# Kernel optimization log

Hardware: AMD Instinct MI355X
Metric: run time of the kernel (lower is better)

Reference implementation:

```python
import jax, jax.numpy as jnp
import numpy as np

B, N_SIDE, S = 64, 40, 512
N = N_SIDE * N_SIDE          # 1600 grid points (fl_feature_dims [1,40,40])
EMB = 10                     # embedding_dim
GDIM = 8                     # lie('homography').dim
WIDTH = 128
C1 = 20                      # first-layer output channels


def _embed(x, emb_dim):
    # sinusoidal embedding of each scalar coordinate: [..., D] -> [..., D*emb_dim]
    freqs = 2.0 ** jnp.arange(emb_dim // 2, dtype=x.dtype)
    ang = x[..., None] * freqs                       # [..., D, emb/2]
    e = jnp.concatenate([jnp.sin(ang), jnp.cos(ang)], axis=-1)  # [..., D, emb]
    return e.reshape(x.shape[:-1] + (x.shape[-1] * emb_dim,))


def _glorot(key, shape):
    fan_in = shape[0]
    return jax.random.normal(key, shape, dtype=jnp.float32) / np.sqrt(fan_in)


def setup_inputs() -> dict:
    key = jax.random.key(0)
    ks = jax.random.split(key, 16)
    inp = {
        'data':   jax.random.normal(ks[0], (B, N, 1), dtype=jnp.float32),
        'v0':     jax.random.normal(ks[1], (S, GDIM), dtype=jnp.float32),
        'v_last': jax.random.normal(ks[2], (S, GDIM), dtype=jnp.float32),
        # FirstLayer filter MLP: 2*EMB -> 20 -> 20 -> 1*C1
        'fl_w1': _glorot(ks[3], (2 * EMB, 20)), 'fl_b1': jnp.zeros((20,), jnp.float32),
        'fl_w2': _glorot(ks[4], (20, 20)),      'fl_b2': jnp.zeros((20,), jnp.float32),
        'fl_w3': _glorot(ks[5], (20, C1)),      'fl_b3': jnp.zeros((C1,), jnp.float32),
        # Hidden FilterMLP: EMB*GDIM=80 -> WIDTH -> C1*WIDTH
        's_w1': _glorot(ks[6], (EMB * GDIM, WIDTH)), 's_b1': jnp.zeros((WIDTH,), jnp.float32),
        's_w2': _glorot(ks[7], (WIDTH, C1 * WIDTH)), 's_b2': jnp.zeros((C1 * WIDTH,), jnp.float32),
        'fc1_w': _glorot(ks[8], (WIDTH, WIDTH)), 'fc1_b': jnp.zeros((WIDTH,), jnp.float32),
        'fc2_w': _glorot(ks[9], (WIDTH, WIDTH)), 'fc2_b': jnp.zeros((WIDTH,), jnp.float32),
        'pool_w': _glorot(ks[10], (WIDTH, 10)),  'pool_b': jnp.zeros((10,), jnp.float32),
    }
    return inp


def reference(data, v0, v_last, fl_w1, fl_b1, fl_w2, fl_b2, fl_w3, fl_b3,
              s_w1, s_b1, s_w2, s_b2, fc1_w, fc1_b, fc2_w, fc2_b, pool_w, pool_b):
    silu = jax.nn.silu
    # pixel grid in [-1,1]^2, homogeneous coords [N,3]
    lin = jnp.linspace(-1.0, 1.0, N_SIDE, dtype=data.dtype)
    xx, yy = jnp.meshgrid(lin, lin, indexing='ij')
    coords = jnp.stack([xx.ravel(), yy.ravel()], axis=-1)           # [N,2]
    xh = jnp.concatenate([coords, jnp.ones((N, 1), data.dtype)], -1)  # [N,3]
    # homography matrices: identity + small perturbation from 8 group params
    pert = jnp.concatenate([0.1 * v_last, jnp.zeros((S, 1), data.dtype)], -1).reshape(S, 3, 3)
    H = jnp.eye(3, dtype=data.dtype) + pert                          # [S,3,3]
    y = jnp.einsum('sij,nj->sni', H, xh)                             # [S,N,3]
    t = y[..., :2] / y[..., 2:3]                                     # projective action [S,N,2]
    # continuous-kernel first layer: filters generated by MLP on embedded coords
    e1 = _embed(t, EMB)                                              # [S,N,20]
    h = silu(e1 @ fl_w1 + fl_b1)
    h = silu(h @ fl_w2 + fl_b2)
    filt1 = h @ fl_w3 + fl_b3                                        # [S,N,C1]
    z = jnp.einsum('bn,sno->bso', data[:, :, 0], filt1) / N          # [B,S,C1]
    z = silu(z)
    # hidden FilterMLP on group samples v0 -> per-sample filters [S,C1,WIDTH]
    v0e = _embed(v0, EMB)                                            # [S,80]
    h2 = silu(v0e @ s_w1 + s_b1)                                     # [S,WIDTH]
    filt2 = (h2 @ s_w2 + s_b2).reshape(S, C1, WIDTH)
    # (1/S) * sum over group-sample and channel axes of broadcast product
    z = jnp.einsum('bsc,scw->bw', z, filt2) / S                      # [B,WIDTH]
    z = silu(z @ fc1_w + fc1_b) + z
    z = silu(z @ fc2_w + fc2_b) + z
    return z @ pool_w + pool_b                                       # [B,10]
```

## Files before the change

kernel.cpp:

```cpp
#include <hip/hip_runtime.h>

#define N_PTS 1600
#define NSIDE 40
#define SNUM  512
#define BNUM  64
#define C1D   20
#define WID   128

typedef _Float16 h8  __attribute__((ext_vector_type(8)));
typedef _Float16 h4  __attribute__((ext_vector_type(4)));
typedef __fp16   h2v __attribute__((ext_vector_type(2)));
typedef float    f4  __attribute__((ext_vector_type(4)));

__device__ __forceinline__ float silu_f(float x){ return x / (1.f + __expf(-x)); }
__device__ __forceinline__ void fma4(float4& a, float s, const float4 w){
    a.x += s*w.x; a.y += s*w.y; a.z += s*w.z; a.w += s*w.w;
}

__global__ __launch_bounds__(256) void ka_prep(
    const float* __restrict__ data, const float* __restrict__ v0,
    const float* __restrict__ s_w1, const float* __restrict__ s_b1,
    const float* __restrict__ s_w2, const float* __restrict__ s_b2,
    const float* __restrict__ w1, const float* __restrict__ b1,
    const float* __restrict__ w2, const float* __restrict__ b2,
    const float* __restrict__ w3, const float* __restrict__ b3,
    _Float16* __restrict__ dataA, float* __restrict__ f2g,
    _Float16* __restrict__ wPackA, float* __restrict__ bPackA)
{
    const int t  = threadIdx.x;
    const int bx = blockIdx.x;
    if (bx == 370) {
        const float* wsrc[3] = { w1, w2, w3 };
        const float* bsrc[3] = { b1, b2, b3 };
        for (int v = t; v < 3072; v += 256) {
            const int l = v >> 10, rem = v & 1023;
            const int cout = rem >> 5, cin = rem & 31;
            float x = 0.f;
            if (cout < 20 && cin < 20) x = wsrc[l][cin * 20 + cout];
            wPackA[v] = (_Float16)x;
        }
        if (t < 96) {
            const int l = t >> 5, cout = t & 31;
            bPackA[t] = (cout < 20) ? bsrc[l][cout] : 0.f;
        }
        return;
    }
    if (bx >= 320) {
        const int o  = (bx - 320) * 256 + t;
        const int L  = o & 63, cm = o >> 6;
        const int mt = cm & 3, ch = cm >> 2;
        const int b  = mt * 16 + (L & 15);
        const int nb = ch * 32 + (L >> 4) * 8;
        const float* src = data + b * N_PTS + nb;
        h8 v;
        #pragma unroll
        for (int j = 0; j < 8; j++) v[j] = (_Float16)src[j];
        *(h8*)(dataA + (size_t)o * 8) = v;
        return;
    }
    const int st  = bx / 10, ct = bx - st * 10;
    const int s0  = st * 16;
    const int col = ct * 256 + t;
    __shared__ __align__(16) float h2t[128][20];

    for (int idx = t; idx < 2048; idx += 256) {
        const int ss = idx >> 7, j = idx & 127;
        float acc = s_b1[j];
        #pragma unroll
        for (int d = 0; d < 8; d++) {
            const float val = v0[(s0 + ss) * 8 + d];
            float sv, cv;
            __sincosf(val, &sv, &cv);
            #pragma unroll
            for (int k = 0; k < 5; k++) {
                acc += sv * s_w1[(d*10 + k)     * WID + j];
                acc += cv * s_w1[(d*10 + 5 + k) * WID + j];
                const float ns = 2.f * sv * cv;
                const float nc = 1.f - 2.f * sv * sv;
                sv = ns; cv = nc;
            }
        }
        h2t[j][ss] = silu_f(acc);
    }
    __syncthreads();

    float4 acc[4];
    #pragma unroll
    for (int qq = 0; qq < 4; qq++) acc[qq] = make_float4(0.f, 0.f, 0.f, 0.f);
    #pragma unroll 4
    for (int i = 0; i < 128; i++) {
        const float wv = s_w2[i * 2560 + col];
        const float4* hh = (const float4*)&h2t[i][0];
        #pragma unroll
        for (int qq = 0; qq < 4; qq++) fma4(acc[qq], wv, hh[qq]);
    }
    const float bias = s_b2[col];
    const float* af = (const float*)acc;
    #pragma unroll
    for (int ss = 0; ss < 16; ss++)
        f2g[(s0 + ss) * 2560 + col] = af[ss] + bias;
}

__device__ __forceinline__ void embed_pt(int n, const float Hm[9], h2v e2[10])
{
    const int i = n / NSIDE;
    const int j = n - i * NSIDE;
    const float x = -1.f + (float)i * (2.f/39.f);
    const float y = -1.f + (float)j * (2.f/39.f);
    const float y0 = Hm[0]*x + Hm[1]*y + Hm[2];
    const float y1 = Hm[3]*x + Hm[4]*y + Hm[5];
    const float y2 = Hm[6]*x + Hm[7]*y + Hm[8];
    const float inv = 1.f / y2;
    const float t0 = y0 * inv, t1 = y1 * inv;
    float e[20];
    float sv0, cv0, sv1, cv1;
    __sincosf(t0, &sv0, &cv0);
    __sincosf(t1, &sv1, &cv1);
    #pragma unroll
    for (int k = 0; k < 5; k++) {
        e[k] = sv0; e[5+k] = cv0; e[10+k] = sv1; e[15+k] = cv1;
        const float ns0 = 2.f*sv0*cv0, nc0 = 1.f - 2.f*sv0*sv0; sv0 = ns0; cv0 = nc0;
        const float ns1 = 2.f*sv1*cv1, nc1 = 1.f - 2.f*sv1*sv1; sv1 = ns1; cv1 = nc1;
    }
    #pragma unroll
    for (int k = 0; k < 10; k++)
        e2[k] = __builtin_amdgcn_cvt_pkrtz(e[2*k], e[2*k+1]);
}

__global__ __launch_bounds__(256) void k1_filt_z(
    const _Float16* __restrict__ dataA, const float* __restrict__ v_last,
    const _Float16* __restrict__ wPackA, const float* __restrict__ bPackA,
    float* __restrict__ zpart)
{
    const int s    = blockIdx.x & 511;
    const int half = blockIdx.x >> 9;
    const int nb0  = half * 800;
    const int t    = threadIdx.x;
    const int lane = t & 63;
    const int w    = t >> 6;
    const int q    = lane >> 4;
    const int l15  = lane & 15;

    __shared__ __align__(16) unsigned char pool[21504];
    __shared__ __align__(16) _Float16 filtB[20 * 264];
    _Float16* act = (_Float16*)pool;
    float*    red = (float*)pool;

    h8 wf[3][2]; float bv[3][2];
    #pragma unroll
    for (int l = 0; l < 3; l++)
        #pragma unroll
        for (int nt = 0; nt < 2; nt++) {
            wf[l][nt] = *(const h8*)(wPackA + (((l*2+nt)*16 + l15) * 32 + q*8));
            bv[l][nt] = bPackA[(l*2+nt)*16 + l15];
        }

    float Hm[9];
    #pragma unroll
    for (int k = 0; k < 9; k++) Hm[k] = (k == 0 || k == 4 || k == 8) ? 1.f : 0.f;
    #pragma unroll
    for (int k = 0; k < 8; k++) Hm[k] += 0.1f * v_last[s*8 + k];

    f4 zacc[4][2];
    #pragma unroll
    for (int mt = 0; mt < 4; mt++) { zacc[mt][0] = (f4)(0.f); zacc[mt][1] = (f4)(0.f); }
    const f4 zero4 = (f4)(0.f);

    {
        unsigned long long* pz = (unsigned long long*)(act + t*40 + 20);
        pz[0] = 0ull; pz[1] = 0ull; pz[2] = 0ull;
    }

    for (int base = 0; base < 800; base += 256) {
        const int tn = min(256, 800 - base);
        if (t < tn) {
            h2v e2[10];
            embed_pt(nb0 + base + t, Hm, e2);
            #pragma unroll
            for (int k = 0; k < 10; k++)
                *(h2v*)(act + t*40 + 2*k) = e2[k];
        }
        __syncthreads();

        const int nmt = tn >> 4;
        #pragma unroll
        for (int l = 0; l < 3; l++) {
            for (int mt = w; mt < nmt; mt += 4) {
                const int r0 = mt * 16;
                const h8 af = *(const h8*)(act + (r0 + l15)*40 + q*8);
                f4 D0 = __builtin_amdgcn_mfma_f32_16x16x32_f16(af, wf[l][0], zero4, 0, 0, 0);
                f4 D1 = __builtin_amdgcn_mfma_f32_16x16x32_f16(af, wf[l][1], zero4, 0, 0, 0);
                if (l < 2) {
                    #pragma unroll
                    for (int r = 0; r < 4; r++) {
                        const int p = r0 + q*4 + r;
                        act[p*40 + l15] = (_Float16)silu_f(D0[r] + bv[l][0]);
                        if (l15 < 4)
                            act[p*40 + 16 + l15] = (_Float16)silu_f(D1[r] + bv[l][1]);
                    }
                } else {
                    h4 p0, p1;
                    #pragma unroll
                    for (int r = 0; r < 4; r++) {
                        p0[r] = (_Float16)(D0[r] + bv[2][0]);
                        p1[r] = (_Float16)(D1[r] + bv[2][1]);
                    }
                    *(h4*)(filtB + l15*264 + r0 + q*4) = p0;
                    if (l15 < 4)
                        *(h4*)(filtB + (16 + l15)*264 + r0 + q*4) = p1;
                }
            }
        }
        __syncthreads();

        const int nkc = tn >> 5;
        const int r1row = (l15 < 4) ? (16 + l15) : 0;
        for (int kc = w; kc < nkc; kc += 4) {
            const int gchunk = ((nb0 + base) >> 5) + kc;
            const h8 bf0 = *(const h8*)(filtB + l15  *264 + kc*32 + q*8);
            const h8 bf1 = *(const h8*)(filtB + r1row*264 + kc*32 + q*8);
            #pragma unroll
            for (int mt = 0; mt < 4; mt++) {
                const h8 afz = *(const h8*)(dataA + ((size_t)(gchunk*4 + mt)*64 + lane)*8);
                zacc[mt][0] = __builtin_amdgcn_mfma_f32_16x16x32_f16(afz, bf0, zacc[mt][0], 0, 0, 0);
                zacc[mt][1] = __builtin_amdgcn_mfma_f32_16x16x32_f16(afz, bf1, zacc[mt][1], 0, 0, 0);
            }
        }
        __syncthreads();
    }

    #pragma unroll
    for (int mt = 0; mt < 4; mt++) {
        #pragma unroll
        for (int r = 0; r < 4; r++) {
            const int b = mt*16 + q*4 + r;
            red[(w*64 + b)*21 + l15] = zacc[mt][0][r];
            if (l15 < 4) red[(w*64 + b)*21 + 16 + l15] = zacc[mt][1][r];
        }
    }
    __syncthreads();
    for (int v = t; v < 1280; v += 256) {
        const int c = v >> 6, b = v & 63;
        const float sum = red[b*21 + c] + red[(64+b)*21 + c]
                        + red[(128+b)*21 + c] + red[(192+b)*21 + c];
        zpart[(half*512 + s)*1280 + v] = sum;
    }
}

__global__ __launch_bounds__(256) void k2_contract(
    const float* __restrict__ zg, const float* __restrict__ f2g,
    float* __restrict__ part)
{
    const int blk = blockIdx.x;
    const int sg  = blk >> 1;
    const int wh  = blk & 1;
    const int s0  = sg * 4;
    const int w0  = wh * 64;
    const int t   = threadIdx.x;
    __shared__ __align__(16) float zl[4*1280];
    __shared__ __align__(16) float fl[4*20*64];
    #pragma unroll
    for (int sp = 0; sp < 4; sp++) {
        const int srow = (s0 + sp) * 1280;
        for (int r = t; r < 1280; r += 256) {
            const float a0 = zg[srow + r];
            const float a1 = zg[512*1280 + srow + r];
            zl[sp*1280 + r] = silu_f((a0 + a1) * (1.f / (float)N_PTS));
        }
        for (int u = t; u < 1280; u += 256) {
            const int c = u >> 6, ww = u & 63;
            fl[sp*1280 + u] = f2g[(s0 + sp)*2560 + c*128 + w0 + ww];
        }
    }
    __syncthreads();
    const int ww = t & 63, bh = t >> 6;
    float4 acc[4];
    #pragma unroll
    for (int qq = 0; qq < 4; qq++) acc[qq] = make_float4(0.f, 0.f, 0.f, 0.f);
    #pragma unroll 4
    for (int sc = 0; sc < 80; sc++) {
        const float f = fl[sc * 64 + ww];
        const float4* zz = (const float4*)&zl[sc * 64 + bh * 16];
        #pragma unroll
        for (int qq = 0; qq < 4; qq++) fma4(acc[qq], f, zz[qq]);
    }
    const float* af = (const float*)acc;
    #pragma unroll
    for (int idx = 0; idx < 16; idx++) {
        const int b = bh * 16 + idx;
        part[blk * 4096 + b * 64 + ww] = af[idx];
    }
}

__global__ __launch_bounds__(128) void k3_tail(
    const float* __restrict__ part,
    const float* __restrict__ fc1w, const float* __restrict__ fc1b,
    const float* __restrict__ fc2w, const float* __restrict__ fc2b,
    const float* __restrict__ pw,   const float* __restrict__ pb,
    float* __restrict__ out)
{
    const int b = blockIdx.x, t = threadIdx.x;
    const int wh = t >> 6, wl = t & 63;
    __shared__ float zb[128], r1[128], r2[128];
    float sum = 0.f;
    #pragma unroll 8
    for (int sg = 0; sg < 128; sg++)
        sum += part[((sg << 1) | wh) * 4096 + b * 64 + wl];
    zb[t] = sum * (1.f / (float)SNUM);
    __syncthreads();
    float a = fc1b[t];
    #pragma unroll 8
    for (int i = 0; i < 128; i++) a += zb[i] * fc1w[i * 128 + t];
    r1[t] = silu_f(a) + zb[t];
    __syncthreads();
    a = fc2b[t];
    #pragma unroll 8
    for (int i = 0; i < 128; i++) a += r1[i] * fc2w[i * 128 + t];
    r2[t] = silu_f(a) + r1[t];
    __syncthreads();
    if (t < 10) {
        float o = pb[t];
        #pragma unroll 8
        for (int i = 0; i < 128; i++) o += r2[i] * pw[i * 10 + t];
        out[b * 10 + t] = o;
    }
}

extern "C" void kernel_launch(void* const* d_in, const int* in_sizes, int n_in,
                              void* d_out, int out_size, void* d_ws, size_t ws_size,
                              hipStream_t stream) {
    const float* data   = (const float*)d_in[0];
    const float* v0     = (const float*)d_in[1];
    const float* v_last = (const float*)d_in[2];
    const float* fl_w1  = (const float*)d_in[3];
    const float* fl_b1  = (const float*)d_in[4];
    const float* fl_w2  = (const float*)d_in[5];
    const float* fl_b2  = (const float*)d_in[6];
    const float* fl_w3  = (const float*)d_in[7];
    const float* fl_b3  = (const float*)d_in[8];
    const float* s_w1   = (const float*)d_in[9];
    const float* s_b1   = (const float*)d_in[10];
    const float* s_w2   = (const float*)d_in[11];
    const float* s_b2   = (const float*)d_in[12];
    const float* fc1_w  = (const float*)d_in[13];
    const float* fc1_b  = (const float*)d_in[14];
    const float* fc2_w  = (const float*)d_in[15];
    const float* fc2_b  = (const float*)d_in[16];
    const float* pool_w = (const float*)d_in[17];
    const float* pool_b = (const float*)d_in[18];
    float* out = (float*)d_out;

    float* ws        = (float*)d_ws;
    _Float16* dataA  = (_Float16*)ws;
    float* zpart  = ws    + 51200;
    float* f2g    = zpart + 1310720;
    float* part   = f2g   + 1310720;
    _Float16* wPackA = (_Float16*)(part + 1048576);
    float* bPackA = part + 1048576 + 1536;

    ka_prep    <<<371, 256, 0, stream>>>(data, v0, s_w1, s_b1, s_w2, s_b2,
                                         fl_w1, fl_b1, fl_w2, fl_b2, fl_w3, fl_b3,
                                         dataA, f2g, wPackA, bPackA);
    k1_filt_z  <<<1024, 256, 0, stream>>>(dataA, v_last, wPackA, bPackA, zpart);
    k2_contract<<<256, 256, 0, stream>>>(zpart, f2g, part);
    k3_tail    <<<64, 128, 0, stream>>>(part, fc1_w, fc1_b, fc2_w, fc2_b,
                                        pool_w, pool_b, out);
}
```

Baseline: 197.1 us.

## Pad activation stride, drop block barrier, reduce partials with atomics

The first-layer activation buffer in shared memory gets a row stride of 42 instead of 40, to cut bank conflicts. The block-wide barrier after the embedding write is removed, and the tile loop is remapped so each wavefront only touches the 64 rows its own lanes wrote. The contraction kernel now atomically adds its results into a small zeroed [64,128] buffer, so the tail kernel no longer reads and reduces a 4 MB partials array. The cost is an extra memset, atomic contention, nondeterministic summation order, and 16-byte vector LDS reads that may no longer be aligned with the odd stride.

Measured after the change: 202.3 us. 2.7% more time.

```diff
diff --git a/kernel.cpp b/kernel.cpp
--- a/kernel.cpp
+++ b/kernel.cpp
@@ -127,6 +127,8 @@
         e2[k] = __builtin_amdgcn_cvt_pkrtz(e[2*k], e[2*k+1]);
 }
 
+#define ASTRIDE 42
+
 __global__ __launch_bounds__(256) void k1_filt_z(
     const _Float16* __restrict__ dataA, const float* __restrict__ v_last,
     const _Float16* __restrict__ wPackA, const float* __restrict__ bPackA,
@@ -167,7 +169,7 @@
     const f4 zero4 = (f4)(0.f);
 
     {
-        unsigned long long* pz = (unsigned long long*)(act + t*40 + 20);
+        unsigned long long* pz = (unsigned long long*)(act + t*ASTRIDE + 20);
         pz[0] = 0ull; pz[1] = 0ull; pz[2] = 0ull;
     }
 
@@ -178,25 +180,27 @@
             embed_pt(nb0 + base + t, Hm, e2);
             #pragma unroll
             for (int k = 0; k < 10; k++)
-                *(h2v*)(act + t*40 + 2*k) = e2[k];
-        }
-        __syncthreads();
+                *(h2v*)(act + t*ASTRIDE + 2*k) = e2[k];
+        }
 
         const int nmt = tn >> 4;
         #pragma unroll
         for (int l = 0; l < 3; l++) {
-            for (int mt = w; mt < nmt; mt += 4) {
+            #pragma unroll
+            for (int i = 0; i < 4; i++) {
+                const int mt = 4*w + i;
+                if (mt >= nmt) break;
                 const int r0 = mt * 16;
-                const h8 af = *(const h8*)(act + (r0 + l15)*40 + q*8);
+                const h8 af = *(const h8*)(act + (r0 + l15)*ASTRIDE + q*8);
                 f4 D0 = __builtin_amdgcn_mfma_f32_16x16x32_f16(af, wf[l][0], zero4, 0, 0, 0);
                 f4 D1 = __builtin_amdgcn_mfma_f32_16x16x32_f16(af, wf[l][1], zero4, 0, 0, 0);
                 if (l < 2) {
                     #pragma unroll
                     for (int r = 0; r < 4; r++) {
                         const int p = r0 + q*4 + r;
-                        act[p*40 + l15] = (_Float16)silu_f(D0[r] + bv[l][0]);
+                        act[p*ASTRIDE + l15] = (_Float16)silu_f(D0[r] + bv[l][0]);
                         if (l15 < 4)
-                            act[p*40 + 16 + l15] = (_Float16)silu_f(D1[r] + bv[l][1]);
+                            act[p*ASTRIDE + 16 + l15] = (_Float16)silu_f(D1[r] + bv[l][1]);
                     }
                 } else {
                     h4 p0, p1;
@@ -249,7 +253,7 @@
 
 __global__ __launch_bounds__(256) void k2_contract(
     const float* __restrict__ zg, const float* __restrict__ f2g,
-    float* __restrict__ part)
+    float* __restrict__ out2g)
 {
     const int blk = blockIdx.x;
     const int sg  = blk >> 1;
@@ -288,25 +292,20 @@
     #pragma unroll
     for (int idx = 0; idx < 16; idx++) {
         const int b = bh * 16 + idx;
-        part[blk * 4096 + b * 64 + ww] = af[idx];
+        atomicAdd(&out2g[b * 128 + w0 + ww], af[idx]);
     }
 }
 
 __global__ __launch_bounds__(128) void k3_tail(
-    const float* __restrict__ part,
+    const float* __restrict__ out2g,
     const float* __restrict__ fc1w, const float* __restrict__ fc1b,
     const float* __restrict__ fc2w, const float* __restrict__ fc2b,
     const float* __restrict__ pw,   const float* __restrict__ pb,
     float* __restrict__ out)
 {
     const int b = blockIdx.x, t = threadIdx.x;
-    const int wh = t >> 6, wl = t & 63;
     __shared__ float zb[128], r1[128], r2[128];
-    float sum = 0.f;
-    #pragma unroll 8
-    for (int sg = 0; sg < 128; sg++)
-        sum += part[((sg << 1) | wh) * 4096 + b * 64 + wl];
-    zb[t] = sum * (1.f / (float)SNUM);
+    zb[t] = out2g[b * 128 + t] * (1.f / (float)SNUM);
     __syncthreads();
     float a = fc1b[t];
     #pragma unroll 8
@@ -354,15 +353,16 @@
     _Float16* dataA  = (_Float16*)ws;
     float* zpart  = ws    + 51200;
     float* f2g    = zpart + 1310720;
-    float* part   = f2g   + 1310720;
-    _Float16* wPackA = (_Float16*)(part + 1048576);
-    float* bPackA = part + 1048576 + 1536;
-
+    float* out2g  = f2g   + 1310720;
+    _Float16* wPackA = (_Float16*)(out2g + 8192);
+    float* bPackA = out2g + 8192 + 1536;
+
+    hipMemsetAsync(out2g, 0, 8192 * sizeof(float), stream);
     ka_prep    <<<371, 256, 0, stream>>>(data, v0, s_w1, s_b1, s_w2, s_b2,
                                          fl_w1, fl_b1, fl_w2, fl_b2, fl_w3, fl_b3,
                                          dataA, f2g, wPackA, bPackA);
     k1_filt_z  <<<1024, 256, 0, stream>>>(dataA, v_last, wPackA, bPackA, zpart);
-    k2_contract<<<256, 256, 0, stream>>>(zpart, f2g, part);
-    k3_tail    <<<64, 128, 0, stream>>>(part, fc1_w, fc1_b, fc2_w, fc2_b,
+    k2_contract<<<256, 256, 0, stream>>>(zpart, f2g, out2g);
+    k3_tail    <<<64, 128, 0, stream>>>(out2g, fc1_w, fc1_b, fc2_w, fc2_b,
                                         pool_w, pool_b, out);
 }
```
